# Performance work log

Hardware: AMD Instinct MI355X
Metric: run time of the kernel (lower is better)

Reference implementation:

```python
import jax, jax.numpy as jnp
import numpy as np

B, K, V, D, H, S, KS = 4, 4, 32, 64, 4, 1024, 5
GROUPS = K * V  # 128


def setup_inputs() -> dict:
    key = jax.random.key(0)
    k1, k2 = jax.random.split(key, 2)
    x = jax.random.normal(k1, (B, GROUPS * 3, S), dtype=jnp.float32)
    # grouped causal conv weight: (out_ch, in_ch_per_group, ks) = (K*V*D*3, 3, KS)
    W = jax.random.normal(k2, (GROUPS * D * 3, 3, KS), dtype=jnp.float32) * 0.05
    b = jnp.zeros((GROUPS * D * 3,), dtype=jnp.float32)
    return {"x": x, "W": W, "b": b}


def reference(x, W, b):
    temperature = 1.0
    dk = D // H
    # --- TCN (stand-in): causal grouped conv1d, groups = K*V ---
    xp = jnp.pad(x, ((0, 0), (0, 0), (KS - 1, 0)))  # left-pad for causality
    y = jax.lax.conv_general_dilated(
        xp, W, window_strides=(1,), padding='VALID',
        dimension_numbers=('NCH', 'OIH', 'NCH'),
        feature_group_count=GROUPS,
    ) + b[None, :, None]                      # (B, K*V*3*D, S)
    # channel layout per group is (3, D) to mirror torch reshape
    y = y.reshape(B * K, V, 3, D, S)
    q, k, v = y[:, :, 0], y[:, :, 1], y[:, :, 2]   # each (BK, V, D, S)
    q = q.reshape(B * K, V, H, dk, S)
    k = k.reshape(B * K, V, H, dk, S)
    v = v.reshape(B * K, V, H, dk, S)
    scale = (dk ** -0.5) / temperature
    # per-timestep attention over variables: (BK, H, S, Vq, Vk)
    logits = jnp.einsum('bqhds,bkhds->bhsqk', q, k) * scale
    attn = jax.nn.softmax(logits, axis=-1)
    # x_out[b,h,s,q,d] = sum_k attn * v  -> permute(0,3,1,4,2) layout (BK,V,H,dk,S)
    xo = jnp.einsum('bhsqk,bkhds->bqhds', attn, v)
    xo = xo.reshape(B * K, V * D, S).reshape(B, K * V * D, S)
    # mean over heads, to (BK, Vq, Vk, S) then (B, K, V, V, S)
    attn_m = jnp.transpose(attn.mean(axis=1), (0, 2, 3, 1)).reshape(B, K, V, V, S)
    return xo, attn_m
```

## Files before the change

### kernel.cpp

```cpp
#include <hip/hip_runtime.h>
#include <hip/hip_bf16.h>
#include <stdint.h>

#define SCALE 0.25f

typedef __attribute__((ext_vector_type(8))) short bf16x8;
typedef __attribute__((ext_vector_type(4))) float f32x4;
typedef __attribute__((ext_vector_type(16))) float f32x16;

__global__ __launch_bounds__(256) void prep_w2_kernel(const float* __restrict__ W,
                                                      float* __restrict__ W2) {
    int idx = blockIdx.x * 256 + threadIdx.x;
    int o = idx >> 4, j = idx & 15;
    W2[idx] = (j < 15) ? W[o * 15 + j] : 0.f;
}

#define LDS_TOTAL 126976

__global__ __launch_bounds__(512, 2) void fused2_kernel(const float* __restrict__ x,
                                                        const float* __restrict__ W2,
                                                        const float* __restrict__ bias,
                                                        float* __restrict__ out,
                                                        float* __restrict__ out_am) {
    extern __shared__ char smraw[];
    float* xs = (float*)smraw;
    char* qkvbuf0 = smraw + 13824;
    char* qkvbuf1 = smraw + 38400;
    float* xobuf0 = (float*)(smraw + 62976);
    float* xobuf1 = (float*)(smraw + 79616);
    unsigned short* vT = (unsigned short*)(smraw + 96256);
    unsigned short* pT = (unsigned short*)(smraw + 106496);
    float* att = (float*)smraw;

    {
    }
    int bi = blockIdx.x, slot = bi & 7, jj = bi >> 3;
    int k_ = slot >> 1, b = jj >> 4, st = ((slot & 1) << 4) | (jj & 15);
    int bk = b * 4 + k_;

    int t = threadIdx.x;
    int wid = t >> 6, lane = t & 63;
    int l31 = lane & 31, hi2 = lane >> 5;
    int l15 = lane & 15, hi4 = lane >> 4;

    {
        int sbase = st * 32 - 4;
        #pragma unroll
        for (int i = 0; i < 7; ++i) {
            int idx = i * 512 + t;
            if (idx < 3456) {
                int row = idx / 36, col = idx - row * 36;
                int sg = sbase + col;
                xs[idx] = (sg >= 0) ? x[((size_t)b * 384 + k_ * 96 + row) * 1024 + sg] : 0.f;
            }
        }
    }

    int v = t >> 4, dk = t & 15;
    int g3 = (k_ * 32 + v) * 3;

    float w[3][16], bs[3];
    auto loadw = [&](int hh) {
        #pragma unroll
        for (int c3 = 0; c3 < 3; ++c3) {
            int row = (g3 + c3) * 64 + hh * 16 + dk;
            const float4* p = (const float4*)(W2 + (size_t)row * 16);
            float4 a0 = p[0], a1 = p[1], a2 = p[2], a3 = p[3];
            w[c3][0] = a0.x;  w[c3][1] = a0.y;  w[c3][2] = a0.z;  w[c3][3] = a0.w;
            w[c3][4] = a1.x;  w[c3][5] = a1.y;  w[c3][6] = a1.z;  w[c3][7] = a1.w;
            w[c3][8] = a2.x;  w[c3][9] = a2.y;  w[c3][10] = a2.z; w[c3][11] = a2.w;
            w[c3][12] = a3.x; w[c3][13] = a3.y; w[c3][14] = a3.z; w[c3][15] = a3.w;
            bs[c3] = bias[row];
        }
    };

    auto conv_stage = [&](int qs, char* dstraw) {
        __hip_bfloat16* dst = (__hip_bfloat16*)dstraw;
        float xw[3][12];
        #pragma unroll
        for (int i = 0; i < 3; ++i)
            #pragma unroll
            for (int j = 0; j < 12; ++j)
                xw[i][j] = xs[(v * 3 + i) * 36 + qs * 8 + j];
        #pragma unroll
        for (int s8 = 0; s8 < 8; ++s8) {
            #pragma unroll
            for (int c3 = 0; c3 < 3; ++c3) {
                float a = bs[c3];
                #pragma unroll
                for (int i = 0; i < 3; ++i)
                    #pragma unroll
                    for (int tt = 0; tt < 5; ++tt)
                        a = fmaf(xw[i][s8 + tt], w[c3][i * 5 + tt], a);
                dst[(s8 * 3 + c3) * 512 + v * 16 + dk] = __float2bfloat16(a);
            }
        }
    };

    auto sweep_stage = [&](int hp, int qp, const float* xo) {
        int c_loc = t;
        int qv = c_loc >> 4, dkc = c_loc & 15;
        int col = c_loc ^ (4 * (qv & 7));
        float o0 = xo[0 * 520 + col], o1 = xo[1 * 520 + col];
        float o2 = xo[2 * 520 + col], o3 = xo[3 * 520 + col];
        float o4 = xo[4 * 520 + col], o5 = xo[5 * 520 + col];
        float o6 = xo[6 * 520 + col], o7 = xo[7 * 520 + col];
        int c = k_ * 2048 + qv * 64 + hp * 16 + dkc;
        float* base = out + ((size_t)b * 8192 + c) * 1024 + st * 32 + qp * 8;
        float4 A; A.x = o0; A.y = o1; A.z = o2; A.w = o3;
        float4 Bv; Bv.x = o4; Bv.y = o5; Bv.z = o6; Bv.w = o7;
        *(float4*)base = A;
        *(float4*)(base + 4) = Bv;
    };

    float acc_am[4][16];
    #pragma unroll
    for (int a = 0; a < 4; ++a)
        #pragma unroll
        for (int r = 0; r < 16; ++r) acc_am[a][r] = 0.f;

    loadw(0);
    __syncthreads();
    conv_stage(0, qkvbuf0);
    __syncthreads();

    for (int h = 0; h < 4; ++h) {
        #pragma unroll
        for (int q = 0; q < 4; ++q) {
            if (q == 3 && h < 3) loadw(h + 1);

            {
                char* qbuf = (q & 1) ? qkvbuf1 : qkvbuf0;
                float* xo = (q & 1) ? xobuf1 : xobuf0;
                const __hip_bfloat16* qb =
                    (const __hip_bfloat16*)qbuf + (wid * 3) * 512 + l31 * 16 + hi2 * 8;
                bf16x8 qf = *(const bf16x8*)qb;
                bf16x8 kf = *(const bf16x8*)(qb + 512);
                uint4 vv = *(const uint4*)(qb + 1024);

                {
                    const unsigned short* us = (const unsigned short*)&vv;
                    #pragma unroll
                    for (int j = 0; j < 8; ++j)
                        vT[(wid * 16 + hi2 * 8 + j) * 40 + l31] = us[j];
                }

                f32x16 zc;
                #pragma unroll
                for (int i = 0; i < 16; ++i) zc[i] = 0.f;
                f32x16 lg = __builtin_amdgcn_mfma_f32_32x32x16_bf16(kf, qf, zc, 0, 0, 0);

                float p[16], m = -3.0e38f;
                #pragma unroll
                for (int r = 0; r < 16; ++r) { p[r] = lg[r] * SCALE; m = fmaxf(m, p[r]); }
                m = fmaxf(m, __shfl_xor(m, 32));
                float ssum = 0.f;
                #pragma unroll
                for (int r = 0; r < 16; ++r) { p[r] = __expf(p[r] - m); ssum += p[r]; }
                ssum += __shfl_xor(ssum, 32);
                float inv = 1.f / ssum;
                #pragma unroll
                for (int r = 0; r < 16; ++r) { p[r] *= inv; acc_am[q][r] += p[r]; }

                unsigned* pTrow = (unsigned*)(pT + (size_t)(wid * 32 + l31) * 40);
                int wsw = (l31 >> 3) & 1 ? 4 : 0;
                #pragma unroll
                for (int mm = 0; mm < 8; ++mm) {
                    unsigned pk;
                    asm("v_cvt_pk_bf16_f32 %0, %1, %2"
                        : "=v"(pk) : "v"(p[2 * mm]), "v"(p[2 * mm + 1]));
                    pTrow[((mm & 1) + 4 * (mm >> 1) + 2 * hi2) ^ wsw] = pk;
                }

                int rsw = (l15 >> 3) & 1 ? 8 : 0;
                bf16x8 vf = *(const bf16x8*)&vT[(wid * 16 + l15) * 40 + hi4 * 8];
                bf16x8 p1 = *(const bf16x8*)&pT[(wid * 32 + l15) * 40 + (hi4 * 8 ^ rsw)];
                bf16x8 p2 = *(const bf16x8*)&pT[(wid * 32 + 16 + l15) * 40 + (hi4 * 8 ^ rsw)];
                f32x4 z4;
                #pragma unroll
                for (int i = 0; i < 4; ++i) z4[i] = 0.f;
                f32x4 xo1 = __builtin_amdgcn_mfma_f32_16x16x32_bf16(vf, p1, z4, 0, 0, 0);
                f32x4 xo2 = __builtin_amdgcn_mfma_f32_16x16x32_bf16(vf, p2, z4, 0, 0, 0);

                float* row = xo + wid * 520;
                int sw = 4 * (l15 & 7);
                *(f32x4*)(row + ((l15 * 16 + hi4 * 4) ^ sw)) = xo1;
                *(f32x4*)(row + (((16 + l15) * 16 + hi4 * 4) ^ sw)) = xo2;
            }

            if (!(h == 3 && q == 3)) {
                conv_stage((q + 1) & 3, ((q + 1) & 1) ? qkvbuf1 : qkvbuf0);
            }

            if (!(h == 0 && q == 0)) {
                int hp = (q == 0) ? h - 1 : h;
                sweep_stage(hp, (q + 3) & 3, ((q + 1) & 1) ? xobuf1 : xobuf0);
            }

            __syncthreads();
        }
    }
    sweep_stage(3, 3, xobuf1);
    __syncthreads();

    #pragma unroll
    for (int pass = 0; pass < 2; ++pass) {
        if (pass) __syncthreads();
        if ((l31 >> 4) == pass) {
            int qh = l31 & 15;
            int csw = 4 * (qh & 7);
            #pragma unroll
            for (int q = 0; q < 4; ++q) {
                int sp = q * 8 + wid;
                int colp = sp ^ csw;
                #pragma unroll
                for (int r = 0; r < 16; ++r) {
                    int kv = (r & 3) + 8 * (r >> 2) + 4 * hi2;
                    att[(qh * 32 + kv) * 36 + colp] = 0.25f * acc_am[q][r];
                }
            }
        }
        __syncthreads();
        #pragma unroll
        for (int j = 0; j < 8; ++j) {
            int tr = j * 64 + (t >> 3);
            int csw = 4 * ((tr >> 5) & 7);
            int s4 = (t & 7) * 4;
            float4 o;
            o.x = att[tr * 36 + ((s4 + 0) ^ csw)];
            o.y = att[tr * 36 + ((s4 + 1) ^ csw)];
            o.z = att[tr * 36 + ((s4 + 2) ^ csw)];
            o.w = att[tr * 36 + ((s4 + 3) ^ csw)];
            *(float4*)(out_am + ((size_t)bk * 1024 + pass * 512 + tr) * 1024 + st * 32 + s4) = o;
        }
    }
}

extern "C" void kernel_launch(void* const* d_in, const int* in_sizes, int n_in,
                              void* d_out, int out_size, void* d_ws, size_t ws_size,
                              hipStream_t stream) {
    const float* x = (const float*)d_in[0];
    const float* W = (const float*)d_in[1];
    const float* bias = (const float*)d_in[2];
    float* out = (float*)d_out;
    float* out_am = out + (size_t)33554432;

    float* W2 = (float*)d_ws;

    (void)hipFuncSetAttribute((const void*)fused2_kernel,
                              hipFuncAttributeMaxDynamicSharedMemorySize, LDS_TOTAL);

    prep_w2_kernel<<<1536, 256, 0, stream>>>(W, W2);
    fused2_kernel<<<512, 512, LDS_TOTAL, stream>>>(x, W2, bias, out, out_am);
}
```

Before: 121.1 us.

## Widen output stores via ring-buffered xo tile and read conv input from global

Replaces the two 8-timestep xo buffers with a 40-row LDS ring buffer. A whole head's 32 timesteps now accumulate before being swept out, so each channel row is written as 128 contiguous bytes instead of 32-byte pieces. The x staging in LDS and its initial sync are dropped, and the conv stage loads float4 windows of x straight from global memory. LDS use grows to about 162KB and x is re-read from global per stage, which trades extra L2 traffic for more coalesced output writes.

Measured after the change: 235.0 us. 1.94x slower.

```diff
diff --git a/kernel.cpp b/kernel.cpp
--- a/kernel.cpp
+++ b/kernel.cpp
@@ -15,25 +15,21 @@
     W2[idx] = (j < 15) ? W[o * 15 + j] : 0.f;
 }
 
-#define LDS_TOTAL 126976
-
-__global__ __launch_bounds__(512, 2) void fused2_kernel(const float* __restrict__ x,
+#define LDS_TOTAL 162112
+
+__global__ __launch_bounds__(512, 2) void fused3_kernel(const float* __restrict__ x,
                                                         const float* __restrict__ W2,
                                                         const float* __restrict__ bias,
                                                         float* __restrict__ out,
                                                         float* __restrict__ out_am) {
     extern __shared__ char smraw[];
-    float* xs = (float*)smraw;
-    char* qkvbuf0 = smraw + 13824;
-    char* qkvbuf1 = smraw + 38400;
-    float* xobuf0 = (float*)(smraw + 62976);
-    float* xobuf1 = (float*)(smraw + 79616);
-    unsigned short* vT = (unsigned short*)(smraw + 96256);
-    unsigned short* pT = (unsigned short*)(smraw + 106496);
+    char* qkvbuf0 = smraw;
+    char* qkvbuf1 = smraw + 24576;
+    float* xo = (float*)(smraw + 49152);
+    unsigned short* vT = (unsigned short*)(smraw + 131392);
+    unsigned short* pT = (unsigned short*)(smraw + 141632);
     float* att = (float*)smraw;
 
-    {
-    }
     int bi = blockIdx.x, slot = bi & 7, jj = bi >> 3;
     int k_ = slot >> 1, b = jj >> 4, st = ((slot & 1) << 4) | (jj & 15);
     int bk = b * 4 + k_;
@@ -42,19 +38,6 @@
     int wid = t >> 6, lane = t & 63;
     int l31 = lane & 31, hi2 = lane >> 5;
     int l15 = lane & 15, hi4 = lane >> 4;
-
-    {
-        int sbase = st * 32 - 4;
-        #pragma unroll
-        for (int i = 0; i < 7; ++i) {
-            int idx = i * 512 + t;
-            if (idx < 3456) {
-                int row = idx / 36, col = idx - row * 36;
-                int sg = sbase + col;
-                xs[idx] = (sg >= 0) ? x[((size_t)b * 384 + k_ * 96 + row) * 1024 + sg] : 0.f;
-            }
-        }
-    }
 
     int v = t >> 4, dk = t & 15;
     int g3 = (k_ * 32 + v) * 3;
@@ -76,12 +59,21 @@
 
     auto conv_stage = [&](int qs, char* dstraw) {
         __hip_bfloat16* dst = (__hip_bfloat16*)dstraw;
-        float xw[3][12];
-        #pragma unroll
-        for (int i = 0; i < 3; ++i)
-            #pragma unroll
-            for (int j = 0; j < 12; ++j)
-                xw[i][j] = xs[(v * 3 + i) * 36 + qs * 8 + j];
+        int idx0 = st * 32 + qs * 8 - 4;
+        float xv[3][12];
+        #pragma unroll
+        for (int i = 0; i < 3; ++i) {
+            const float* xr = x + ((size_t)b * 384 + k_ * 96 + v * 3 + i) * 1024;
+            #pragma unroll
+            for (int wq = 0; wq < 3; ++wq) {
+                int s0 = idx0 + wq * 4;
+                float4 f;
+                if (s0 >= 0) f = *(const float4*)(xr + s0);
+                else { f.x = 0.f; f.y = 0.f; f.z = 0.f; f.w = 0.f; }
+                xv[i][wq * 4 + 0] = f.x; xv[i][wq * 4 + 1] = f.y;
+                xv[i][wq * 4 + 2] = f.z; xv[i][wq * 4 + 3] = f.w;
+            }
+        }
         #pragma unroll
         for (int s8 = 0; s8 < 8; ++s8) {
             #pragma unroll
@@ -91,26 +83,30 @@
                 for (int i = 0; i < 3; ++i)
                     #pragma unroll
                     for (int tt = 0; tt < 5; ++tt)
-                        a = fmaf(xw[i][s8 + tt], w[c3][i * 5 + tt], a);
+                        a = fmaf(xv[i][s8 + tt], w[c3][i * 5 + tt], a);
                 dst[(s8 * 3 + c3) * 512 + v * 16 + dk] = __float2bfloat16(a);
             }
         }
     };
 
-    auto sweep_stage = [&](int hp, int qp, const float* xo) {
-        int c_loc = t;
-        int qv = c_loc >> 4, dkc = c_loc & 15;
-        int col = c_loc ^ (4 * (qv & 7));
-        float o0 = xo[0 * 520 + col], o1 = xo[1 * 520 + col];
-        float o2 = xo[2 * 520 + col], o3 = xo[3 * 520 + col];
-        float o4 = xo[4 * 520 + col], o5 = xo[5 * 520 + col];
-        float o6 = xo[6 * 520 + col], o7 = xo[7 * 520 + col];
-        int c = k_ * 2048 + qv * 64 + hp * 16 + dkc;
-        float* base = out + ((size_t)b * 8192 + c) * 1024 + st * 32 + qp * 8;
-        float4 A; A.x = o0; A.y = o1; A.z = o2; A.w = o3;
-        float4 Bv; Bv.x = o4; Bv.y = o5; Bv.z = o6; Bv.w = o7;
-        *(float4*)base = A;
-        *(float4*)(base + 4) = Bv;
+    auto sweep = [&](int hp) {
+        int rb = (32 * hp) % 40;
+        int u = t >> 3;
+        int s4 = (t & 7) * 4;
+        #pragma unroll
+        for (int j = 0; j < 8; ++j) {
+            int c_loc = j * 64 + u;
+            int col = c_loc ^ (4 * ((c_loc >> 4) & 7));
+            float4 o;
+            #pragma unroll
+            for (int i2 = 0; i2 < 4; ++i2) {
+                int r = rb + s4 + i2; if (r >= 40) r -= 40;
+                (&o.x)[i2] = xo[r * 514 + col];
+            }
+            int qv = c_loc >> 4, dkc = c_loc & 15;
+            int c = k_ * 2048 + qv * 64 + hp * 16 + dkc;
+            *(float4*)(out + ((size_t)b * 8192 + c) * 1024 + st * 32 + s4) = o;
+        }
     };
 
     float acc_am[4][16];
@@ -120,7 +116,6 @@
         for (int r = 0; r < 16; ++r) acc_am[a][r] = 0.f;
 
     loadw(0);
-    __syncthreads();
     conv_stage(0, qkvbuf0);
     __syncthreads();
 
@@ -131,7 +126,6 @@
 
             {
                 char* qbuf = (q & 1) ? qkvbuf1 : qkvbuf0;
-                float* xo = (q & 1) ? xobuf1 : xobuf0;
                 const __hip_bfloat16* qb =
                     (const __hip_bfloat16*)qbuf + (wid * 3) * 512 + l31 * 16 + hi2 * 8;
                 bf16x8 qf = *(const bf16x8*)qb;
@@ -182,7 +176,8 @@
                 f32x4 xo1 = __builtin_amdgcn_mfma_f32_16x16x32_bf16(vf, p1, z4, 0, 0, 0);
                 f32x4 xo2 = __builtin_amdgcn_mfma_f32_16x16x32_bf16(vf, p2, z4, 0, 0, 0);
 
-                float* row = xo + wid * 520;
+                int rr = (32 * h + 8 * q + wid) % 40;
+                float* row = xo + rr * 514;
                 int sw = 4 * (l15 & 7);
                 *(f32x4*)(row + ((l15 * 16 + hi4 * 4) ^ sw)) = xo1;
                 *(f32x4*)(row + (((16 + l15) * 16 + hi4 * 4) ^ sw)) = xo2;
@@ -192,15 +187,12 @@
                 conv_stage((q + 1) & 3, ((q + 1) & 1) ? qkvbuf1 : qkvbuf0);
             }
 
-            if (!(h == 0 && q == 0)) {
-                int hp = (q == 0) ? h - 1 : h;
-                sweep_stage(hp, (q + 3) & 3, ((q + 1) & 1) ? xobuf1 : xobuf0);
-            }
+            if (q == 0 && h > 0) sweep(h - 1);
 
             __syncthreads();
         }
     }
-    sweep_stage(3, 3, xobuf1);
+    sweep(3);
     __syncthreads();
 
     #pragma unroll
@@ -247,9 +239,9 @@
 
     float* W2 = (float*)d_ws;
 
-    (void)hipFuncSetAttribute((const void*)fused2_kernel,
+    (void)hipFuncSetAttribute((const void*)fused3_kernel,
                               hipFuncAttributeMaxDynamicSharedMemorySize, LDS_TOTAL);
 
     prep_w2_kernel<<<1536, 256, 0, stream>>>(W, W2);
-    fused2_kernel<<<512, 512, LDS_TOTAL, stream>>>(x, W2, bias, out, out_am);
+    fused3_kernel<<<512, 512, LDS_TOTAL, stream>>>(x, W2, bias, out, out_am);
 }
```
